# Optimization experiments

Measured on AMD Instinct MI355X. Metric: run time of the kernel, lower is better.

Reference implementation:

```python
import jax, jax.numpy as jnp
import numpy as np

U_NUM = 100000
I_NUM = 50000
D = 64
E = 4_000_000
N_LAYERS = 3


def setup_inputs() -> dict:
    key = jax.random.key(0)
    k1, k2, k3, k4 = jax.random.split(key, 4)
    return {
        "user_emb": jax.random.normal(k1, (U_NUM + 1, D), dtype=jnp.float32) * 0.1,
        "item_emb": jax.random.normal(k2, (I_NUM + 1, D), dtype=jnp.float32) * 0.1,
        "edge_user": jax.random.randint(k3, (E,), 0, U_NUM + 1, dtype=jnp.int32),
        "edge_item": jax.random.randint(k4, (E,), 0, I_NUM + 1, dtype=jnp.int32),
    }


def reference(user_emb, item_emb, edge_user, edge_item):
    U = user_emb.shape[0]
    I = item_emb.shape[0]
    N = U + I
    # Symmetrize bipartite interaction edges into full-graph COO indices.
    rows = jnp.concatenate([edge_user, edge_item + U])          # [2E]
    cols = jnp.concatenate([edge_item + U, edge_user])          # [2E]
    # Symmetric degree normalization: A_hat = D^-1/2 A D^-1/2 (deg + 1e-7)
    deg = jax.ops.segment_sum(jnp.ones(rows.shape[0], dtype=jnp.float32), rows, num_segments=N) + 1e-7
    d_inv_sqrt = deg ** -0.5
    vals = d_inv_sqrt[rows] * d_inv_sqrt[cols]                  # [2E]

    emb = jnp.concatenate([user_emb, item_emb], axis=0)         # [N, D]
    acc = emb
    x = emb
    for _ in range(N_LAYERS):
        # SpMM: x_new[r] = sum_{edges (r,c)} vals * x[c]
        x = jax.ops.segment_sum(vals[:, None] * x[cols], rows, num_segments=N)
        acc = acc + x
    total = acc / jnp.float32(N_LAYERS + 1)                     # mean over layer stack
    return total[:U], total[U:]
```

## Files before the change

### kernel.cpp

```cpp
#include <hip/hip_runtime.h>


static constexpr int D = 64;
#define BSHIFT 8
#define BROWS 256
#define KP 1024
#define TILE 2048
#define PADSLACK (7 * BROWS)
#define CSR_LDS_CAP 12288
#define COLS_SLACK 8192

__device__ __forceinline__ float bflo(unsigned v) {
    unsigned u = v << 16;
    return __builtin_bit_cast(float, u);
}
__device__ __forceinline__ float bfhi(unsigned v) {
    unsigned u = v & 0xFFFF0000u;
    return __builtin_bit_cast(float, u);
}
__device__ __forceinline__ unsigned pack_bf16x2(float a, float b) {
    unsigned ua = __builtin_bit_cast(unsigned, a);
    unsigned ub = __builtin_bit_cast(unsigned, b);
    ua += 0x7FFFu + ((ua >> 16) & 1u);
    ub += 0x7FFFu + ((ub >> 16) & 1u);
    return (ua >> 16) | (ub & 0xFFFF0000u);
}
__device__ __forceinline__ unsigned pack_f16x2(float a, float b) {
    unsigned short ua = __builtin_bit_cast(unsigned short, (_Float16)a);
    unsigned short ub = __builtin_bit_cast(unsigned short, (_Float16)b);
    return (unsigned)ua | ((unsigned)ub << 16);
}
__device__ __forceinline__ float f16lo(unsigned v) {
    return (float)__builtin_bit_cast(_Float16, (unsigned short)(v & 0xFFFFu));
}
__device__ __forceinline__ float f16hi(unsigned v) {
    return (float)__builtin_bit_cast(_Float16, (unsigned short)(v >> 16));
}

__device__ __forceinline__ void acc_bf2(unsigned u, float& se, float& so) {
    se += bflo(u);
    so += bfhi(u);
}

__global__ __launch_bounds__(256) void bucket_count(
        const int* __restrict__ eu, const int* __restrict__ ei,
        int* __restrict__ bcnt, int E, int U) {
    __shared__ int h[KP];
    int tid = threadIdx.x;
#pragma unroll
    for (int k = 0; k < 4; ++k) h[tid + k * 256] = 0;
    __syncthreads();
    int E4 = E >> 2;
    int stride = gridDim.x * blockDim.x;
    int g = blockIdx.x * blockDim.x + tid;
    const int4* eu4 = (const int4*)eu;
    const int4* ei4 = (const int4*)ei;
    for (int e = g; e < E4; e += stride) {
        int4 u = eu4[e];
        int4 it = ei4[e];
        atomicAdd(&h[u.x >> BSHIFT], 1);
        atomicAdd(&h[u.y >> BSHIFT], 1);
        atomicAdd(&h[u.z >> BSHIFT], 1);
        atomicAdd(&h[u.w >> BSHIFT], 1);
        atomicAdd(&h[(U + it.x) >> BSHIFT], 1);
        atomicAdd(&h[(U + it.y) >> BSHIFT], 1);
        atomicAdd(&h[(U + it.z) >> BSHIFT], 1);
        atomicAdd(&h[(U + it.w) >> BSHIFT], 1);
    }
    if (blockIdx.x == 0 && tid < (E - (E4 << 2))) {
        int e = (E4 << 2) + tid;
        atomicAdd(&h[eu[e] >> BSHIFT], 1);
        atomicAdd(&h[(U + ei[e]) >> BSHIFT], 1);
    }
    __syncthreads();
#pragma unroll
    for (int k = 0; k < 4; ++k) {
        int v = h[tid + k * 256];
        if (v) atomicAdd(&bcnt[tid + k * 256], v);
    }
}

__global__ void bscan(const int* __restrict__ bcnt, int* __restrict__ bbase,
                      int* __restrict__ bcursor, int KB, int twoE) {
    __shared__ int s[KP];
    int tid = threadIdx.x;
    int v = (tid < KB) ? bcnt[tid] : 0;
    s[tid] = v;
    __syncthreads();
    for (int off = 1; off < KP; off <<= 1) {
        int a = (tid >= off) ? s[tid - off] : 0;
        __syncthreads();
        s[tid] += a;
        __syncthreads();
    }
    int ex = s[tid] - v;
    if (tid < KB) { bbase[tid] = ex; bcursor[tid] = ex; }
    if (tid == KB) bbase[tid] = twoE;
    if (tid > KB) bcursor[tid] = 0;
}

__global__ __launch_bounds__(256) void bucket_scatter(
        const int* __restrict__ eu, const int* __restrict__ ei,
        int* __restrict__ bcursor, unsigned* __restrict__ pairs,
        int E, int U, int twoE) {
    __shared__ int hist[KP];
    __shared__ int sbase[KP];
    __shared__ int gbase[KP];
    __shared__ unsigned staging[TILE];
    __shared__ unsigned short sb[TILE];
    int tid = threadIdx.x;
#pragma unroll
    for (int k = 0; k < 4; ++k) hist[tid + k * 256] = 0;
    __syncthreads();
    int base_e = blockIdx.x * TILE;
    int bk[8]; unsigned pk[8];
#pragma unroll
    for (int k = 0; k < 8; ++k) {
        int e = base_e + k * 256 + tid;
        bk[k] = -1;
        if (e < twoE) {
            int r, c;
            if (e < E) { r = eu[e]; c = U + ei[e]; }
            else       { c = eu[e - E]; r = U + ei[e - E]; }
            int b = r >> BSHIFT;
            bk[k] = b;
            pk[k] = ((unsigned)(r & (BROWS - 1)) << 18) | (unsigned)c;
            atomicAdd(&hist[b], 1);
        }
    }
    __syncthreads();
    int cc[4];
#pragma unroll
    for (int k = 0; k < 4; ++k) cc[k] = hist[tid + k * 256];
    for (int off = 1; off < KP; off <<= 1) {
        int a[4];
#pragma unroll
        for (int k = 0; k < 4; ++k) {
            int idx = tid + k * 256;
            a[k] = (idx >= off) ? hist[idx - off] : 0;
        }
        __syncthreads();
#pragma unroll
        for (int k = 0; k < 4; ++k) hist[tid + k * 256] += a[k];
        __syncthreads();
    }
#pragma unroll
    for (int k = 0; k < 4; ++k) {
        int idx = tid + k * 256;
        int e0 = hist[idx] - cc[k];
        sbase[idx] = e0;
        if (cc[k] > 0) gbase[idx] = atomicAdd(&bcursor[idx], cc[k]);
        hist[idx] = e0;
    }
    __syncthreads();
#pragma unroll
    for (int k = 0; k < 8; ++k) {
        if (bk[k] >= 0) {
            int pos = atomicAdd(&hist[bk[k]], 1);
            staging[pos] = pk[k];
            sb[pos] = (unsigned short)bk[k];
        }
    }
    __syncthreads();
    int tile_n = min(TILE, twoE - base_e);
#pragma unroll
    for (int k = 0; k < 8; ++k) {
        int j = k * 256 + tid;
        if (j < tile_n) {
            int b = sb[j];
            pairs[gbase[b] + (j - sbase[b])] = staging[j];
        }
    }
}

__global__ __launch_bounds__(256) void csr_build(
        const unsigned* __restrict__ pairs, const int* __restrict__ bbase,
        int* __restrict__ deg, int* __restrict__ row_ptr, float* __restrict__ dis,
        int* __restrict__ cols, int N) {
    __shared__ int cnt[BROWS];
    __shared__ int cur[BROWS];
    __shared__ int fin[BROWS];
    __shared__ int lbuf[CSR_LDS_CAP];
    __shared__ int meta[2];
    int tid = threadIdx.x;
    int b = blockIdx.x;
    int lo = bbase[b], hi = bbase[b + 1];
    int cbase = lo + PADSLACK * b;
    cnt[tid] = 0;
    __syncthreads();
    for (int i = lo + tid; i < hi; i += 256) atomicAdd(&cnt[pairs[i] >> 18], 1);
    __syncthreads();
    int c = cnt[tid];
    int p = (c + 7) & ~7;
    cnt[tid] = p;
    __syncthreads();
    for (int off = 1; off < BROWS; off <<= 1) {
        int a = (tid >= off) ? cnt[tid - off] : 0;
        __syncthreads();
        cnt[tid] += a;
        __syncthreads();
    }
    int e = cnt[tid] - p;
    int r = (b << BSHIFT) + tid;
    if (r < N) {
        deg[r] = c;
        row_ptr[r] = cbase + e;
        dis[r] = rsqrtf((float)c + 1e-7f);
    }
    cur[tid] = e;
    fin[tid] = e + p;
    if (tid == 127) meta[0] = cnt[127];
    if (tid == 255) meta[1] = cnt[255];
    __syncthreads();
    int half0 = meta[0];
    int total = meta[1];
    if (half0 <= CSR_LDS_CAP && (total - half0) <= CSR_LDS_CAP) {
#pragma unroll
        for (int half = 0; half < 2; ++half) {
            int base = half ? half0 : 0;
            int end  = half ? total : half0;
            for (int i = lo + tid; i < hi; i += 256) {
                unsigned pe = pairs[i];
                int row = (int)(pe >> 18);
                if ((row >> 7) == half) {
                    int pos = atomicAdd(&cur[row], 1);
                    lbuf[pos - base] = (int)(pe & 0x3FFFFu);
                }
            }
            __syncthreads();
            if ((tid >> 7) == half) {
                for (int i = cur[tid]; i < fin[tid]; ++i) lbuf[i - base] = N;
            }
            __syncthreads();
            for (int i = base + tid; i < end; i += 256)
                cols[cbase + i] = lbuf[i - base];
            __syncthreads();
        }
    } else {
        for (int i = lo + tid; i < hi; i += 256) {
            unsigned pe = pairs[i];
            int pos = atomicAdd(&cur[pe >> 18], 1);
            cols[cbase + pos] = (int)(pe & 0x3FFFFu);
        }
        __syncthreads();
        for (int i = cur[tid]; i < fin[tid]; ++i) cols[cbase + i] = N;
    }
}

__global__ __launch_bounds__(256) void init_kernel(
        const float4* __restrict__ ue4, const float4* __restrict__ ie4,
        const float* __restrict__ dis,
        uint4* __restrict__ xsA4, uint4* __restrict__ xsB4,
        int U8, int N8) {
    int t = blockIdx.x * blockDim.x + threadIdx.x;
    if (t >= N8 + 8) return;
    if (t >= N8) {
        uint4 z = {0u, 0u, 0u, 0u};
        xsA4[t] = z;
        xsB4[t] = z;
        return;
    }
    float dv = dis[t >> 3];
    const float4* src = (t < U8) ? (ue4 + 2 * t) : (ie4 + 2 * (t - U8));
    float4 a0 = src[0];
    float4 a1 = src[1];
    uint4 w;
    w.x = pack_bf16x2(dv * a0.x, dv * a0.y);
    w.y = pack_bf16x2(dv * a0.z, dv * a0.w);
    w.z = pack_bf16x2(dv * a1.x, dv * a1.y);
    w.w = pack_bf16x2(dv * a1.z, dv * a1.w);
    xsA4[t] = w;
}

__global__ __launch_bounds__(256) void spmm_mid(
        const int* __restrict__ row_ptr, const int* __restrict__ deg,
        const float* __restrict__ dis, const int* __restrict__ cols,
        const unsigned* __restrict__ xs, unsigned* __restrict__ xs_next,
        unsigned* __restrict__ xh, int N) {
    int wid = blockIdx.x * 4 + (threadIdx.x >> 6);
    if (wid >= N) return;
    int lane = threadIdx.x & 63;
    int n8 = lane >> 3;
    int dp = lane & 7;
    int start = row_ptr[wid];
    int cntp = (deg[wid] + 7) & ~7;
    float dr = dis[wid];
    const int* colp = cols + start;
    int vbase = n8 << 2;
    int dpo = dp << 2;
    float s0 = 0.f, s1 = 0.f, s2 = 0.f, s3 = 0.f;
    float s4 = 0.f, s5 = 0.f, s6 = 0.f, s7 = 0.f;
    for (int chunk = 0; chunk < cntp; chunk += 64) {
        int cv = colp[chunk + lane];
        int nq = min(64, cntp - chunk) >> 3;
        nq = __builtin_amdgcn_readfirstlane(nq);
        int coq[8];
        uint4 vq[8];
#pragma unroll
        for (int q = 0; q < 8; ++q) {
            if (q < nq)
                coq[q] = __builtin_amdgcn_ds_bpermute((q << 5) + vbase, cv);
        }
#pragma unroll
        for (int q = 0; q < 8; ++q) {
            if (q < nq)
                vq[q] = *(const uint4*)(xs + (((unsigned)coq[q]) << 5) + dpo);
        }
#pragma unroll
        for (int q = 0; q < 8; ++q) {
            if (q < nq) {
                acc_bf2(vq[q].x, s0, s1);
                acc_bf2(vq[q].y, s2, s3);
                acc_bf2(vq[q].z, s4, s5);
                acc_bf2(vq[q].w, s6, s7);
            }
        }
    }
#pragma unroll
    for (int m = 8; m < 64; m <<= 1) {
        s0 += __shfl_xor(s0, m); s1 += __shfl_xor(s1, m);
        s2 += __shfl_xor(s2, m); s3 += __shfl_xor(s3, m);
        s4 += __shfl_xor(s4, m); s5 += __shfl_xor(s5, m);
        s6 += __shfl_xor(s6, m); s7 += __shfl_xor(s7, m);
    }
    if (n8 == 0) {
        float x0 = dr * s0, x1 = dr * s1, x2 = dr * s2, x3 = dr * s3;
        float x4 = dr * s4, x5 = dr * s5, x6 = dr * s6, x7 = dr * s7;
        uint4 w;
        w.x = pack_bf16x2(dr * x0, dr * x1);
        w.y = pack_bf16x2(dr * x2, dr * x3);
        w.z = pack_bf16x2(dr * x4, dr * x5);
        w.w = pack_bf16x2(dr * x6, dr * x7);
        ((uint4*)xs_next)[(wid << 3) + dp] = w;
        uint4 h;
        h.x = pack_f16x2(x0, x1);
        h.y = pack_f16x2(x2, x3);
        h.z = pack_f16x2(x4, x5);
        h.w = pack_f16x2(x6, x7);
        ((uint4*)xh)[(wid << 3) + dp] = h;
    }
}

__global__ __launch_bounds__(256) void spmm_last(
        const int* __restrict__ row_ptr, const int* __restrict__ deg,
        const float* __restrict__ dis, const int* __restrict__ cols,
        const unsigned* __restrict__ xs,
        const float4* __restrict__ ue4, const float4* __restrict__ ie4,
        const unsigned* __restrict__ xh1, const unsigned* __restrict__ xh2,
        float4* __restrict__ out4, int U, int N) {
    int wid = blockIdx.x * 4 + (threadIdx.x >> 6);
    if (wid >= N) return;
    int lane = threadIdx.x & 63;
    int n8 = lane >> 3;
    int dp = lane & 7;
    int start = row_ptr[wid];
    int cntp = (deg[wid] + 7) & ~7;
    float dr = dis[wid];
    const int* colp = cols + start;
    int vbase = n8 << 2;
    int dpo = dp << 2;
    float s0 = 0.f, s1 = 0.f, s2 = 0.f, s3 = 0.f;
    float s4 = 0.f, s5 = 0.f, s6 = 0.f, s7 = 0.f;
    for (int chunk = 0; chunk < cntp; chunk += 64) {
        int cv = colp[chunk + lane];
        int nq = min(64, cntp - chunk) >> 3;
        nq = __builtin_amdgcn_readfirstlane(nq);
        int coq[8];
        uint4 vq[8];
#pragma unroll
        for (int q = 0; q < 8; ++q) {
            if (q < nq)
                coq[q] = __builtin_amdgcn_ds_bpermute((q << 5) + vbase, cv);
        }
#pragma unroll
        for (int q = 0; q < 8; ++q) {
            if (q < nq)
                vq[q] = *(const uint4*)(xs + (((unsigned)coq[q]) << 5) + dpo);
        }
#pragma unroll
        for (int q = 0; q < 8; ++q) {
            if (q < nq) {
                acc_bf2(vq[q].x, s0, s1);
                acc_bf2(vq[q].y, s2, s3);
                acc_bf2(vq[q].z, s4, s5);
                acc_bf2(vq[q].w, s6, s7);
            }
        }
    }
#pragma unroll
    for (int m = 8; m < 64; m <<= 1) {
        s0 += __shfl_xor(s0, m); s1 += __shfl_xor(s1, m);
        s2 += __shfl_xor(s2, m); s3 += __shfl_xor(s3, m);
        s4 += __shfl_xor(s4, m); s5 += __shfl_xor(s5, m);
        s6 += __shfl_xor(s6, m); s7 += __shfl_xor(s7, m);
    }
    if (n8 == 0) {
        float x30 = dr * s0, x31 = dr * s1, x32 = dr * s2, x33 = dr * s3;
        float x34 = dr * s4, x35 = dr * s5, x36 = dr * s6, x37 = dr * s7;
        const float4* ep = (wid < U) ? (ue4 + (size_t)wid * 16)
                                     : (ie4 + (size_t)(wid - U) * 16);
        float4 e0 = ep[2 * dp];
        float4 e1 = ep[2 * dp + 1];
        uint4 h1 = ((const uint4*)xh1)[(wid << 3) + dp];
        uint4 h2 = ((const uint4*)xh2)[(wid << 3) + dp];
        float4 o0, o1;
        o0.x = 0.25f * (e0.x + f16lo(h1.x) + f16lo(h2.x) + x30);
        o0.y = 0.25f * (e0.y + f16hi(h1.x) + f16hi(h2.x) + x31);
        o0.z = 0.25f * (e0.z + f16lo(h1.y) + f16lo(h2.y) + x32);
        o0.w = 0.25f * (e0.w + f16hi(h1.y) + f16hi(h2.y) + x33);
        o1.x = 0.25f * (e1.x + f16lo(h1.z) + f16lo(h2.z) + x34);
        o1.y = 0.25f * (e1.y + f16hi(h1.z) + f16hi(h2.z) + x35);
        o1.z = 0.25f * (e1.z + f16lo(h1.w) + f16lo(h2.w) + x36);
        o1.w = 0.25f * (e1.w + f16hi(h1.w) + f16hi(h2.w) + x37);
        int oo = (wid << 4) + (dp << 1);
        out4[oo] = o0;
        out4[oo + 1] = o1;
    }
}

extern "C" void kernel_launch(void* const* d_in, const int* in_sizes, int n_in,
                              void* d_out, int out_size, void* d_ws, size_t ws_size,
                              hipStream_t stream) {
    const float* ue = (const float*)d_in[0];
    const float* ie = (const float*)d_in[1];
    const int* eu = (const int*)d_in[2];
    const int* ei = (const int*)d_in[3];
    const int U = in_sizes[0] / D;
    const int I = in_sizes[1] / D;
    const int N = U + I;
    const int E = in_sizes[2];
    const int twoE = 2 * E;
    const int KB = (N + BROWS - 1) / BROWS;
    float* out = (float*)d_out;

    char* ws = (char*)d_ws;
    auto alloc = [&](size_t bytes) {
        char* p = ws;
        ws += (bytes + 255) & ~(size_t)255;
        return p;
    };
    int* deg = (int*)alloc((size_t)N * 4);
    int* row_ptr = (int*)alloc((size_t)N * 4);
    float* dis = (float*)alloc((size_t)N * 4);
    int* bcnt = (int*)alloc(KP * 4);
    int* bbase = (int*)alloc((KP + 1) * 4);
    int* bcursor = (int*)alloc(KP * 4);
    int* cols = (int*)alloc(((size_t)twoE + (size_t)PADSLACK * (KB + 1) + COLS_SLACK) * 4);
    unsigned* pairs = (unsigned*)alloc((size_t)twoE * 4);
    unsigned* xsA = (unsigned*)alloc(((size_t)N + 1) * 32 * 4);
    unsigned* xsB = (unsigned*)alloc(((size_t)N + 1) * 32 * 4);
    unsigned* xh1 = pairs;
    unsigned* xh2 = (unsigned*)alloc((size_t)N * 32 * 4);

    hipMemsetAsync(bcnt, 0, KP * 4, stream);
    bucket_count<<<1024, 256, 0, stream>>>(eu, ei, bcnt, E, U);
    bscan<<<1, KP, 0, stream>>>(bcnt, bbase, bcursor, KB, twoE);
    bucket_scatter<<<(twoE + TILE - 1) / TILE, 256, 0, stream>>>(
        eu, ei, bcursor, pairs, E, U, twoE);
    csr_build<<<KB, BROWS, 0, stream>>>(pairs, bbase, deg, row_ptr, dis, cols, N);

    int N8 = N * 8, U8 = U * 8;
    init_kernel<<<(N8 + 8 + 255) / 256, 256, 0, stream>>>(
        (const float4*)ue, (const float4*)ie, dis,
        (uint4*)xsA, (uint4*)xsB, U8, N8);

    int nblocks = (N + 3) / 4;
    spmm_mid<<<nblocks, 256, 0, stream>>>(
        row_ptr, deg, dis, cols, xsA, xsB, xh1, N);
    spmm_mid<<<nblocks, 256, 0, stream>>>(
        row_ptr, deg, dis, cols, xsB, xsA, xh2, N);
    spmm_last<<<nblocks, 256, 0, stream>>>(
        row_ptr, deg, dis, cols, xsA,
        (const float4*)ue, (const float4*)ie, xh1, xh2, (float4*)out, U, N);
}
```

Measured before the change: 620.1 us.

## Count per-row degrees globally and simplify CSR build into single LDS pass

The bucket histogram is replaced by a per-row global atomic degree count, and the bucket totals are derived by summing degrees in the scan kernel. csr_build then reads degrees directly, dropping its counting pass over pairs and the two-half LDS staging in favour of one LDS buffer. The scatter tile doubles to 4096 edges per block. The cost is 8M global atomics on the degree array instead of LDS atomics, and a serial 256-element sum per thread in the single-block scan.

```diff
diff --git a/kernel.cpp b/kernel.cpp
--- a/kernel.cpp
+++ b/kernel.cpp
@@ -5,9 +5,10 @@
 #define BSHIFT 8
 #define BROWS 256
 #define KP 1024
-#define TILE 2048
+#define TILE 4096
+#define TK 16
 #define PADSLACK (7 * BROWS)
-#define CSR_LDS_CAP 12288
+#define FULL_CAP 16384
 #define COLS_SLACK 8192
 
 __device__ __forceinline__ float bflo(unsigned v) {
@@ -42,49 +43,49 @@
     so += bfhi(u);
 }
 
-__global__ __launch_bounds__(256) void bucket_count(
+__global__ __launch_bounds__(256) void deg_count(
         const int* __restrict__ eu, const int* __restrict__ ei,
-        int* __restrict__ bcnt, int E, int U) {
-    __shared__ int h[KP];
-    int tid = threadIdx.x;
-#pragma unroll
-    for (int k = 0; k < 4; ++k) h[tid + k * 256] = 0;
-    __syncthreads();
+        int* __restrict__ deg, int E, int U) {
     int E4 = E >> 2;
     int stride = gridDim.x * blockDim.x;
-    int g = blockIdx.x * blockDim.x + tid;
+    int g = blockIdx.x * blockDim.x + threadIdx.x;
     const int4* eu4 = (const int4*)eu;
     const int4* ei4 = (const int4*)ei;
     for (int e = g; e < E4; e += stride) {
         int4 u = eu4[e];
         int4 it = ei4[e];
-        atomicAdd(&h[u.x >> BSHIFT], 1);
-        atomicAdd(&h[u.y >> BSHIFT], 1);
-        atomicAdd(&h[u.z >> BSHIFT], 1);
-        atomicAdd(&h[u.w >> BSHIFT], 1);
-        atomicAdd(&h[(U + it.x) >> BSHIFT], 1);
-        atomicAdd(&h[(U + it.y) >> BSHIFT], 1);
-        atomicAdd(&h[(U + it.z) >> BSHIFT], 1);
-        atomicAdd(&h[(U + it.w) >> BSHIFT], 1);
-    }
-    if (blockIdx.x == 0 && tid < (E - (E4 << 2))) {
-        int e = (E4 << 2) + tid;
-        atomicAdd(&h[eu[e] >> BSHIFT], 1);
-        atomicAdd(&h[(U + ei[e]) >> BSHIFT], 1);
-    }
-    __syncthreads();
-#pragma unroll
-    for (int k = 0; k < 4; ++k) {
-        int v = h[tid + k * 256];
-        if (v) atomicAdd(&bcnt[tid + k * 256], v);
-    }
-}
-
-__global__ void bscan(const int* __restrict__ bcnt, int* __restrict__ bbase,
-                      int* __restrict__ bcursor, int KB, int twoE) {
+        atomicAdd(&deg[u.x], 1);
+        atomicAdd(&deg[u.y], 1);
+        atomicAdd(&deg[u.z], 1);
+        atomicAdd(&deg[u.w], 1);
+        atomicAdd(&deg[U + it.x], 1);
+        atomicAdd(&deg[U + it.y], 1);
+        atomicAdd(&deg[U + it.z], 1);
+        atomicAdd(&deg[U + it.w], 1);
+    }
+    if (blockIdx.x == 0 && threadIdx.x < (E - (E4 << 2))) {
+        int e = (E4 << 2) + threadIdx.x;
+        atomicAdd(&deg[eu[e]], 1);
+        atomicAdd(&deg[U + ei[e]], 1);
+    }
+}
+
+__global__ void bscan(const int* __restrict__ deg, int* __restrict__ bbase,
+                      int* __restrict__ bcursor, int KB, int N, int twoE) {
     __shared__ int s[KP];
     int tid = threadIdx.x;
-    int v = (tid < KB) ? bcnt[tid] : 0;
+    int v = 0;
+    if (tid < KB) {
+        int r0 = tid << BSHIFT;
+        int r1 = min(r0 + BROWS, N);
+        const int4* d4 = (const int4*)(deg + r0);
+        int nfull = (r1 - r0) >> 2;
+        for (int k = 0; k < nfull; ++k) {
+            int4 q = d4[k];
+            v += q.x + q.y + q.z + q.w;
+        }
+        for (int i = r0 + (nfull << 2); i < r1; ++i) v += deg[i];
+    }
     s[tid] = v;
     __syncthreads();
     for (int off = 1; off < KP; off <<= 1) {
@@ -113,9 +114,9 @@
     for (int k = 0; k < 4; ++k) hist[tid + k * 256] = 0;
     __syncthreads();
     int base_e = blockIdx.x * TILE;
-    int bk[8]; unsigned pk[8];
-#pragma unroll
-    for (int k = 0; k < 8; ++k) {
+    int bk[TK]; unsigned pk[TK];
+#pragma unroll
+    for (int k = 0; k < TK; ++k) {
         int e = base_e + k * 256 + tid;
         bk[k] = -1;
         if (e < twoE) {
@@ -154,7 +155,7 @@
     }
     __syncthreads();
 #pragma unroll
-    for (int k = 0; k < 8; ++k) {
+    for (int k = 0; k < TK; ++k) {
         if (bk[k] >= 0) {
             int pos = atomicAdd(&hist[bk[k]], 1);
             staging[pos] = pk[k];
@@ -164,7 +165,7 @@
     __syncthreads();
     int tile_n = min(TILE, twoE - base_e);
 #pragma unroll
-    for (int k = 0; k < 8; ++k) {
+    for (int k = 0; k < TK; ++k) {
         int j = k * 256 + tid;
         if (j < tile_n) {
             int b = sb[j];
@@ -175,22 +176,17 @@
 
 __global__ __launch_bounds__(256) void csr_build(
         const unsigned* __restrict__ pairs, const int* __restrict__ bbase,
-        int* __restrict__ deg, int* __restrict__ row_ptr, float* __restrict__ dis,
-        int* __restrict__ cols, int N) {
+        const int* __restrict__ deg, int* __restrict__ row_ptr,
+        float* __restrict__ dis, int* __restrict__ cols, int N) {
     __shared__ int cnt[BROWS];
     __shared__ int cur[BROWS];
-    __shared__ int fin[BROWS];
-    __shared__ int lbuf[CSR_LDS_CAP];
-    __shared__ int meta[2];
+    __shared__ int lbuf[FULL_CAP];
     int tid = threadIdx.x;
     int b = blockIdx.x;
     int lo = bbase[b], hi = bbase[b + 1];
     int cbase = lo + PADSLACK * b;
-    cnt[tid] = 0;
-    __syncthreads();
-    for (int i = lo + tid; i < hi; i += 256) atomicAdd(&cnt[pairs[i] >> 18], 1);
-    __syncthreads();
-    int c = cnt[tid];
+    int r = (b << BSHIFT) + tid;
+    int c = (r < N) ? deg[r] : 0;
     int p = (c + 7) & ~7;
     cnt[tid] = p;
     __syncthreads();
@@ -201,41 +197,24 @@
         __syncthreads();
     }
     int e = cnt[tid] - p;
-    int r = (b << BSHIFT) + tid;
     if (r < N) {
-        deg[r] = c;
         row_ptr[r] = cbase + e;
         dis[r] = rsqrtf((float)c + 1e-7f);
     }
     cur[tid] = e;
-    fin[tid] = e + p;
-    if (tid == 127) meta[0] = cnt[127];
-    if (tid == 255) meta[1] = cnt[255];
-    __syncthreads();
-    int half0 = meta[0];
-    int total = meta[1];
-    if (half0 <= CSR_LDS_CAP && (total - half0) <= CSR_LDS_CAP) {
-#pragma unroll
-        for (int half = 0; half < 2; ++half) {
-            int base = half ? half0 : 0;
-            int end  = half ? total : half0;
-            for (int i = lo + tid; i < hi; i += 256) {
-                unsigned pe = pairs[i];
-                int row = (int)(pe >> 18);
-                if ((row >> 7) == half) {
-                    int pos = atomicAdd(&cur[row], 1);
-                    lbuf[pos - base] = (int)(pe & 0x3FFFFu);
-                }
-            }
-            __syncthreads();
-            if ((tid >> 7) == half) {
-                for (int i = cur[tid]; i < fin[tid]; ++i) lbuf[i - base] = N;
-            }
-            __syncthreads();
-            for (int i = base + tid; i < end; i += 256)
-                cols[cbase + i] = lbuf[i - base];
-            __syncthreads();
-        }
+    int total = cnt[BROWS - 1];
+    __syncthreads();
+    if (total <= FULL_CAP) {
+        for (int i = lo + tid; i < hi; i += 256) {
+            unsigned pe = pairs[i];
+            int pos = atomicAdd(&cur[pe >> 18], 1);
+            lbuf[pos] = (int)(pe & 0x3FFFFu);
+        }
+        __syncthreads();
+        for (int i = e + c; i < e + p; ++i) lbuf[i] = N;
+        __syncthreads();
+        for (int i = tid; i < total; i += 256)
+            cols[cbase + i] = lbuf[i];
     } else {
         for (int i = lo + tid; i < hi; i += 256) {
             unsigned pe = pairs[i];
@@ -243,7 +222,7 @@
             cols[cbase + pos] = (int)(pe & 0x3FFFFu);
         }
         __syncthreads();
-        for (int i = cur[tid]; i < fin[tid]; ++i) cols[cbase + i] = N;
+        for (int i = e + c; i < e + p; ++i) cols[cbase + i] = N;
     }
 }
 
@@ -442,7 +421,6 @@
     int* deg = (int*)alloc((size_t)N * 4);
     int* row_ptr = (int*)alloc((size_t)N * 4);
     float* dis = (float*)alloc((size_t)N * 4);
-    int* bcnt = (int*)alloc(KP * 4);
     int* bbase = (int*)alloc((KP + 1) * 4);
     int* bcursor = (int*)alloc(KP * 4);
     int* cols = (int*)alloc(((size_t)twoE + (size_t)PADSLACK * (KB + 1) + COLS_SLACK) * 4);
@@ -452,9 +430,9 @@
     unsigned* xh1 = pairs;
     unsigned* xh2 = (unsigned*)alloc((size_t)N * 32 * 4);
 
-    hipMemsetAsync(bcnt, 0, KP * 4, stream);
-    bucket_count<<<1024, 256, 0, stream>>>(eu, ei, bcnt, E, U);
-    bscan<<<1, KP, 0, stream>>>(bcnt, bbase, bcursor, KB, twoE);
+    hipMemsetAsync(deg, 0, (size_t)N * 4, stream);
+    deg_count<<<1024, 256, 0, stream>>>(eu, ei, deg, E, U);
+    bscan<<<1, KP, 0, stream>>>(deg, bbase, bcursor, KB, N, twoE);
     bucket_scatter<<<(twoE + TILE - 1) / TILE, 256, 0, stream>>>(
         eu, ei, bcursor, pairs, E, U, twoE);
     csr_build<<<KB, BROWS, 0, stream>>>(pairs, bbase, deg, row_ptr, dis, cols, N);
```

Measured after the change: 883.6 us. +42.5%, slower.
